# Kernel tuning notes

Hardware: AMD Instinct MI355X
Metric: run time of the kernel (lower is better)

Reference implementation:

```python
import jax, jax.numpy as jnp
import numpy as np

K_VALUES = (2, 4, 8)  # sorted k_values from init


def setup_inputs() -> dict:
    key = jax.random.key(0)
    ks = jax.random.split(key, 6)
    B, T, D, H = 16, 2048, 512, 64
    nk = len(K_VALUES)
    # columns: (E, Pt, eta, phi) -- E,Pt positive, eta in [-3,3], phi in [-pi,pi]
    u = jax.random.uniform(ks[0], (B, T, 4), jnp.float32)
    tokens_cont = u * jnp.array([100.0, 50.0, 6.0, 6.2832], jnp.float32) + jnp.array([1.0, 1.0, -3.0, -3.1416], jnp.float32)
    lengths = jax.random.randint(ks[1], (B,), T // 2, T + 1)
    mask = jnp.arange(T)[None, :] < lengths[:, None]  # [B,T] True=valid
    W1 = jax.random.normal(ks[2], (nk, H), jnp.float32) / np.sqrt(nk).astype(np.float32)
    b1 = jax.random.normal(ks[3], (H,), jnp.float32) * 0.01
    W2 = jax.random.normal(ks[4], (H, D), jnp.float32) / np.sqrt(H).astype(np.float32)
    b2 = jax.random.normal(ks[5], (D,), jnp.float32) * 0.01
    return dict(tokens_cont=tokens_cont, mask=mask, W1=W1, b1=b1, W2=W2, b2=b2)


def reference(tokens_cont, mask, W1, b1, W2, b2):
    B, T, _ = tokens_cont.shape
    E, Pt, eta, phi = (tokens_cont[..., i] for i in range(4))
    px = Pt * jnp.cos(phi)
    py = Pt * jnp.sin(phi)
    pz = Pt * jnp.sinh(jnp.clip(eta, -20.0, 20.0))
    P = jnp.stack([E, px, py, pz], axis=-1)  # [B,T,4] four-momentum
    metric = jnp.array([1.0, -1.0, -1.0, -1.0], P.dtype)
    # Lorentz dot: E_i E_j - px_i px_j - py_i py_j - pz_i pz_j -> [B,T,T]
    dot = jnp.einsum('btc,bsc->bts', P * metric, P)
    dot = jnp.where(mask[:, None, :], dot, -jnp.inf)  # exclude padding friends
    max_k = min(max(K_VALUES), T)
    _, topk_idx = jax.lax.top_k(dot, max_k)  # [B,T,max_k]
    Pf = P[jnp.arange(B)[:, None, None], topk_idx]  # gather friends [B,T,max_k,4]
    cum = jnp.cumsum(Pf, axis=2)  # prefix sums over sorted friends
    masses = []
    maskf = mask.astype(P.dtype)
    for k in K_VALUES:
        ps = cum[:, :, min(k, max_k) - 1, :]  # [B,T,4] summed 4-momentum of top-k group
        m2 = ps[..., 0] ** 2 - jnp.sum(ps[..., 1:] ** 2, axis=-1)
        m2 = jnp.maximum(m2, 0.0) * maskf
        masses.append(jnp.sqrt(m2 + 1e-8))
    mass = jnp.stack(masses, axis=-1)  # [B,T,n_k]
    h = jax.nn.gelu(mass @ W1 + b1, approximate=False)  # torch GELU = exact erf
    return h @ W2 + b2  # [B,T,model_dim]
```

## Files before the change

kernel.cpp:

```cpp
#include <hip/hip_runtime.h>
#include <hip/hip_bf16.h>
#include <math.h>

#define NB 16
#define NT 2048
#define ND 512
#define NH 64

typedef __attribute__((ext_vector_type(8))) short short8;
typedef __attribute__((ext_vector_type(4))) float float4v;

__device__ __forceinline__ bool mask_is_bytes(const int* m) {
    return m[0] == 0x01010101;
}
__device__ __forceinline__ bool mask_at(const int* m, bool bytes, int i) {
    if (bytes) return ((const unsigned char*)m)[i] != 0;
    return m[i] != 0;
}

__device__ __forceinline__ float dot4(float4 a, float4 p) {
    float d = a.x * p.x;
    d = __builtin_fmaf(a.y, p.y, d);
    d = __builtin_fmaf(a.z, p.z, d);
    d = __builtin_fmaf(a.w, p.w, d);
    return d;
}

__device__ __forceinline__ unsigned short f2bf(float x) {
    unsigned int u = __float_as_uint(x);
    u += 0x7fffu + ((u >> 16) & 1u);
    return (unsigned short)(u >> 16);
}

__global__ void __launch_bounds__(256) w2t_kernel(
        const float* __restrict__ W2, unsigned short* __restrict__ W2t) {
    int i = blockIdx.x * 256 + threadIdx.x;
    int n = i & (ND - 1), k = i >> 9;
    W2t[n * NH + k] = f2bf(W2[k * ND + n]);
}

#define VT(w2, j, l)  scratch[((w2) * 8 + (j)) * 64 + (l)]
#define PS(w2, c, l)  scratch[((w2) * 12 + (c)) * 64 + (l)]

__global__ void __launch_bounds__(512) fused_topk_mass_mlp_kernel(
        const float* __restrict__ tok,
        const int* __restrict__ mask,
        const float* __restrict__ W1,
        const float* __restrict__ b1,
        const unsigned short* __restrict__ W2t,
        const float* __restrict__ b2,
        float* __restrict__ out) {
    __shared__ float Plds[NT * 4];
    __shared__ float scratch[8 * 12 * 64];
    __shared__ unsigned short hs[64][88];
    __shared__ float mass_s[3][64];
    __shared__ int wcnt[8];

    const int b    = blockIdx.y;
    const int t0   = blockIdx.x * 64;
    const int tid  = threadIdx.x;
    const int lane = tid & 63;
    const int w    = tid >> 6;
    const bool mb  = mask_is_bytes(mask);

    const bool blockValid = mask_at(mask, mb, b * NT + t0);

    if (blockValid) {
        int cnt = 0;
#pragma unroll
        for (int it = 0; it < 4; ++it) {
            int i = tid + it * 512;
            float4 tv = ((const float4*)tok)[b * NT + i];
            bool m = mask_at(mask, mb, b * NT + i);
            float E = tv.x, Pt = tv.y, eta = tv.z, phi = tv.w;
            float px = Pt * cosf(phi);
            float py = Pt * sinf(phi);
            float pz = Pt * sinhf(fminf(fmaxf(eta, -20.f), 20.f));
            float4 pv = m ? make_float4(E, px, py, pz)
                          : make_float4(-1e30f, 0.f, 0.f, 0.f);
            *(float4*)&Plds[i * 4] = pv;
            cnt += (int)__popcll(__ballot(m));
        }
        if (lane == 0) wcnt[w] = cnt;
        __syncthreads();

        int L = 0;
#pragma unroll
        for (int j = 0; j < 8; ++j) L += wcnt[j];
        const int C    = (L + 7) >> 3;
        const int sBeg = w * C;
        const int sEnd = min(sBeg + C, L);

        float4 pt = *(const float4*)&Plds[(t0 + lane) * 4];
        float4 a  = make_float4(pt.x, -pt.y, -pt.z, -pt.w);

        const float NEGBIG = -3.402823466e38f;
        float v0 = NEGBIG, v1 = NEGBIG, v2 = NEGBIG, v3 = NEGBIG;
        float v4 = NEGBIG, v5 = NEGBIG, v6 = NEGBIG, v7 = NEGBIG;

#pragma unroll 4
        for (int s = sBeg; s < sEnd; ++s) {
            float4 ps = *(const float4*)&Plds[s * 4];
            float d = dot4(a, ps);
            float n0 = fmaxf(v0, d);
            float n1 = __builtin_amdgcn_fmed3f(d, v0, v1);
            float n2 = __builtin_amdgcn_fmed3f(d, v1, v2);
            float n3 = __builtin_amdgcn_fmed3f(d, v2, v3);
            float n4 = __builtin_amdgcn_fmed3f(d, v3, v4);
            float n5 = __builtin_amdgcn_fmed3f(d, v4, v5);
            float n6 = __builtin_amdgcn_fmed3f(d, v5, v6);
            float n7 = __builtin_amdgcn_fmed3f(d, v6, v7);
            v0 = n0; v1 = n1; v2 = n2; v3 = n3;
            v4 = n4; v5 = n5; v6 = n6; v7 = n7;
        }
        VT(w, 0, lane) = v0; VT(w, 1, lane) = v1;
        VT(w, 2, lane) = v2; VT(w, 3, lane) = v3;
        VT(w, 4, lane) = v4; VT(w, 5, lane) = v5;
        VT(w, 6, lane) = v6; VT(w, 7, lane) = v7;
        __syncthreads();

        float m0 = NEGBIG, m1 = NEGBIG, m2_ = NEGBIG, m3 = NEGBIG;
        float m4 = NEGBIG, m5 = NEGBIG, m6 = NEGBIG, m7 = NEGBIG;
#pragma unroll
        for (int w2 = 0; w2 < 8; ++w2) {
#pragma unroll
            for (int j = 0; j < 8; ++j) {
                float d = VT(w2, j, lane);
                float n0 = fmaxf(m0, d);
                float n1 = __builtin_amdgcn_fmed3f(d, m0, m1);
                float n2 = __builtin_amdgcn_fmed3f(d, m1, m2_);
                float n3 = __builtin_amdgcn_fmed3f(d, m2_, m3);
                float n4 = __builtin_amdgcn_fmed3f(d, m3, m4);
                float n5 = __builtin_amdgcn_fmed3f(d, m4, m5);
                float n6 = __builtin_amdgcn_fmed3f(d, m5, m6);
                float n7 = __builtin_amdgcn_fmed3f(d, m6, m7);
                m0 = n0; m1 = n1; m2_ = n2; m3 = n3;
                m4 = n4; m5 = n5; m6 = n6; m7 = n7;
            }
        }
        const float th2 = m1, th4 = m3, th8 = m7;
        __syncthreads();

        float s2x = 0.f, s2y = 0.f, s2z = 0.f, s2w = 0.f;
        float s4x = 0.f, s4y = 0.f, s4z = 0.f, s4w = 0.f;
        float s8x = 0.f, s8y = 0.f, s8z = 0.f, s8w = 0.f;
#pragma unroll 4
        for (int s = sBeg; s < sEnd; ++s) {
            float4 ps = *(const float4*)&Plds[s * 4];
            float d = dot4(a, ps);
            if (d >= th8) {
                s8x += ps.x; s8y += ps.y; s8z += ps.z; s8w += ps.w;
                if (d >= th4) {
                    s4x += ps.x; s4y += ps.y; s4z += ps.z; s4w += ps.w;
                    if (d >= th2) {
                        s2x += ps.x; s2y += ps.y; s2z += ps.z; s2w += ps.w;
                    }
                }
            }
        }
        PS(w, 0, lane) = s2x;  PS(w, 1, lane) = s2y;
        PS(w, 2, lane) = s2z;  PS(w, 3, lane) = s2w;
        PS(w, 4, lane) = s4x;  PS(w, 5, lane) = s4y;
        PS(w, 6, lane) = s4z;  PS(w, 7, lane) = s4w;
        PS(w, 8, lane) = s8x;  PS(w, 9, lane) = s8y;
        PS(w, 10, lane) = s8z; PS(w, 11, lane) = s8w;
        __syncthreads();

        if (w == 0) {
            float tot[12];
#pragma unroll
            for (int c = 0; c < 12; ++c) {
                float acc = 0.f;
#pragma unroll
                for (int w2 = 0; w2 < 8; ++w2) acc += PS(w2, c, lane);
                tot[c] = acc;
            }
            const bool maskt = (t0 + lane) < L;
            const float MZ = sqrtf(1e-8f);
            auto massf = [&](float sx, float sy, float sz, float sw) -> float {
                float q = sx * sx;
                q = __builtin_fmaf(-sy, sy, q);
                q = __builtin_fmaf(-sz, sz, q);
                q = __builtin_fmaf(-sw, sw, q);
                q = fmaxf(q, 0.f);
                return sqrtf(q + 1e-8f);
            };
            mass_s[0][lane] = maskt ? massf(tot[0], tot[1], tot[2], tot[3]) : MZ;
            mass_s[1][lane] = maskt ? massf(tot[4], tot[5], tot[6], tot[7]) : MZ;
            mass_s[2][lane] = maskt ? massf(tot[8], tot[9], tot[10], tot[11]) : MZ;
        }
    } else {
        if (tid < 64) {
            const float MZ = sqrtf(1e-8f);
            mass_s[0][tid] = MZ;
            mass_s[1][tid] = MZ;
            mass_s[2][tid] = MZ;
        }
    }
    __syncthreads();

    {
        const int tt = lane;
        const int hr = w;
        float q0 = mass_s[0][tt];
        float q1 = mass_s[1][tt];
        float q2 = mass_s[2][tt];
        unsigned short hv[8];
#pragma unroll
        for (int j = 0; j < 8; ++j) {
            int hh = hr * 8 + j;
            float pre = b1[hh];
            pre = __builtin_fmaf(q0, W1[hh], pre);
            pre = __builtin_fmaf(q1, W1[NH + hh], pre);
            pre = __builtin_fmaf(q2, W1[2 * NH + hh], pre);
            float g = 0.5f * pre * (1.0f + erff(pre * 0.70710678118654752f));
            hv[j] = f2bf(g);
        }
        *(short8*)&hs[tt][hr * 8] = *(const short8*)hv;
    }
    __syncthreads();

    const int col   = lane & 15;
    const int quad  = lane >> 4;
    const int mhalf = w >> 2;
    const int nBase = (w & 3) * 128;

    short8 afrag[2][2];
#pragma unroll
    for (int mt = 0; mt < 2; ++mt)
#pragma unroll
        for (int ks = 0; ks < 2; ++ks)
            afrag[mt][ks] = *(const short8*)&hs[mhalf * 32 + mt * 16 + col][ks * 32 + quad * 8];

    float4v acc[2][8];
#pragma unroll
    for (int mt = 0; mt < 2; ++mt)
#pragma unroll
        for (int nt = 0; nt < 8; ++nt)
            acc[mt][nt] = (float4v)(0.f);

#pragma unroll
    for (int nt = 0; nt < 8; ++nt) {
        const unsigned short* wp = W2t + (nBase + nt * 16 + col) * NH + quad * 8;
        short8 bf0 = *(const short8*)(wp);
        short8 bf1 = *(const short8*)(wp + 32);
        acc[0][nt] = __builtin_amdgcn_mfma_f32_16x16x32_bf16(afrag[0][0], bf0, acc[0][nt], 0, 0, 0);
        acc[1][nt] = __builtin_amdgcn_mfma_f32_16x16x32_bf16(afrag[1][0], bf0, acc[1][nt], 0, 0, 0);
        acc[0][nt] = __builtin_amdgcn_mfma_f32_16x16x32_bf16(afrag[0][1], bf1, acc[0][nt], 0, 0, 0);
        acc[1][nt] = __builtin_amdgcn_mfma_f32_16x16x32_bf16(afrag[1][1], bf1, acc[1][nt], 0, 0, 0);
    }

#pragma unroll
    for (int nt = 0; nt < 8; ++nt) {
        float bias = b2[nBase + nt * 16 + col];
#pragma unroll
        for (int mt = 0; mt < 2; ++mt) {
            int mRow = b * NT + t0 + mhalf * 32 + mt * 16 + quad * 4;
            size_t base = (size_t)mRow * ND + nBase + nt * 16 + col;
#pragma unroll
            for (int r = 0; r < 4; ++r) {
                out[base + (size_t)r * ND] = acc[mt][nt][r] + bias;
            }
        }
    }
}

extern "C" void kernel_launch(void* const* d_in, const int* in_sizes, int n_in,
                              void* d_out, int out_size, void* d_ws, size_t ws_size,
                              hipStream_t stream) {
    const float* tok  = (const float*)d_in[0];
    const int*   mask = (const int*)d_in[1];
    const float* W1   = (const float*)d_in[2];
    const float* b1   = (const float*)d_in[3];
    const float* W2   = (const float*)d_in[4];
    const float* b2   = (const float*)d_in[5];
    float*       out  = (float*)d_out;

    unsigned short* W2t = (unsigned short*)d_ws;

    w2t_kernel<<<dim3(ND * NH / 256), dim3(256), 0, stream>>>(W2, W2t);

    dim3 gB(NT / 64, NB);
    fused_topk_mass_mlp_kernel<<<gB, dim3(512), 0, stream>>>(
        tok, mask, W1, b1, W2t, b2, out);
}
```

Before: 134.6 us.

## Precompute four-momenta in prep kernel and stream friends from global memory

The four-momentum conversion (cos, sin, sinh) moves out of the fused kernel into a prep kernel that also transposes W2, and the result is written once to workspace. The fused kernel drops its 32KB LDS buffer and reads friend momenta from global memory with wave-uniform (readfirstlane) indices, so those loads can become scalar loads. This removes the per-block recomputation of transcendentals for all 2048 tokens and frees LDS, which may raise occupancy. It adds a global round trip and makes the inner loops depend on scalar cache bandwidth. The first top-k loop's unroll also goes from 4 to 8.

Result: slower. 163.6 us (+21.5%).

```diff
diff --git a/kernel.cpp b/kernel.cpp
--- a/kernel.cpp
+++ b/kernel.cpp
@@ -32,25 +32,39 @@
     return (unsigned short)(u >> 16);
 }
 
-__global__ void __launch_bounds__(256) w2t_kernel(
-        const float* __restrict__ W2, unsigned short* __restrict__ W2t) {
+__global__ void __launch_bounds__(256) prep_kernel(
+        const float* __restrict__ tok, const int* __restrict__ mask,
+        const float* __restrict__ W2, unsigned short* __restrict__ W2t,
+        float4* __restrict__ Pg) {
     int i = blockIdx.x * 256 + threadIdx.x;
-    int n = i & (ND - 1), k = i >> 9;
-    W2t[n * NH + k] = f2bf(W2[k * ND + n]);
+    if (i < ND * NH) {
+        int n = i & (ND - 1), k = i >> 9;
+        W2t[n * NH + k] = f2bf(W2[k * ND + n]);
+    } else {
+        int j = i - ND * NH;
+        const bool mb = mask_is_bytes(mask);
+        float4 tv = ((const float4*)tok)[j];
+        bool m = mask_at(mask, mb, j);
+        float E = tv.x, Pt = tv.y, eta = tv.z, phi = tv.w;
+        float px = Pt * cosf(phi);
+        float py = Pt * sinf(phi);
+        float pz = Pt * sinhf(fminf(fmaxf(eta, -20.f), 20.f));
+        Pg[j] = m ? make_float4(E, px, py, pz)
+                  : make_float4(-1e30f, 0.f, 0.f, 0.f);
+    }
 }
 
 #define VT(w2, j, l)  scratch[((w2) * 8 + (j)) * 64 + (l)]
 #define PS(w2, c, l)  scratch[((w2) * 12 + (c)) * 64 + (l)]
 
 __global__ void __launch_bounds__(512) fused_topk_mass_mlp_kernel(
-        const float* __restrict__ tok,
         const int* __restrict__ mask,
         const float* __restrict__ W1,
         const float* __restrict__ b1,
         const unsigned short* __restrict__ W2t,
         const float* __restrict__ b2,
+        const float4* __restrict__ Pg,
         float* __restrict__ out) {
-    __shared__ float Plds[NT * 4];
     __shared__ float scratch[8 * 12 * 64];
     __shared__ unsigned short hs[64][88];
     __shared__ float mass_s[3][64];
@@ -70,15 +84,7 @@
 #pragma unroll
         for (int it = 0; it < 4; ++it) {
             int i = tid + it * 512;
-            float4 tv = ((const float4*)tok)[b * NT + i];
             bool m = mask_at(mask, mb, b * NT + i);
-            float E = tv.x, Pt = tv.y, eta = tv.z, phi = tv.w;
-            float px = Pt * cosf(phi);
-            float py = Pt * sinf(phi);
-            float pz = Pt * sinhf(fminf(fmaxf(eta, -20.f), 20.f));
-            float4 pv = m ? make_float4(E, px, py, pz)
-                          : make_float4(-1e30f, 0.f, 0.f, 0.f);
-            *(float4*)&Plds[i * 4] = pv;
             cnt += (int)__popcll(__ballot(m));
         }
         if (lane == 0) wcnt[w] = cnt;
@@ -91,16 +97,17 @@
         const int sBeg = w * C;
         const int sEnd = min(sBeg + C, L);
 
-        float4 pt = *(const float4*)&Plds[(t0 + lane) * 4];
+        const float4* Pb = Pg + (size_t)b * NT;
+        float4 pt = Pb[t0 + lane];
         float4 a  = make_float4(pt.x, -pt.y, -pt.z, -pt.w);
 
         const float NEGBIG = -3.402823466e38f;
         float v0 = NEGBIG, v1 = NEGBIG, v2 = NEGBIG, v3 = NEGBIG;
         float v4 = NEGBIG, v5 = NEGBIG, v6 = NEGBIG, v7 = NEGBIG;
 
-#pragma unroll 4
+#pragma unroll 8
         for (int s = sBeg; s < sEnd; ++s) {
-            float4 ps = *(const float4*)&Plds[s * 4];
+            float4 ps = Pb[__builtin_amdgcn_readfirstlane(s)];
             float d = dot4(a, ps);
             float n0 = fmaxf(v0, d);
             float n1 = __builtin_amdgcn_fmed3f(d, v0, v1);
@@ -146,7 +153,7 @@
         float s8x = 0.f, s8y = 0.f, s8z = 0.f, s8w = 0.f;
 #pragma unroll 4
         for (int s = sBeg; s < sEnd; ++s) {
-            float4 ps = *(const float4*)&Plds[s * 4];
+            float4 ps = Pb[__builtin_amdgcn_readfirstlane(s)];
             float d = dot4(a, ps);
             if (d >= th8) {
                 s8x += ps.x; s8y += ps.y; s8z += ps.z; s8w += ps.w;
@@ -277,10 +284,12 @@
     float*       out  = (float*)d_out;
 
     unsigned short* W2t = (unsigned short*)d_ws;
-
-    w2t_kernel<<<dim3(ND * NH / 256), dim3(256), 0, stream>>>(W2, W2t);
+    float4*         Pg  = (float4*)((char*)d_ws + 0x10000);
+
+    prep_kernel<<<dim3((ND * NH + NB * NT) / 256), dim3(256), 0, stream>>>(
+        tok, mask, W2, W2t, Pg);
 
     dim3 gB(NT / 64, NB);
     fused_topk_mass_mlp_kernel<<<gB, dim3(512), 0, stream>>>(
-        tok, mask, W1, b1, W2t, b2, out);
-}
+        mask, W1, b1, W2t, b2, Pg, out);
+}
```
